# Kernel tuning notes

Measured on AMD Instinct MI355X. Metric: run time of the kernel, lower is better.

The kernel has to match this reference:

```python
import jax, jax.numpy as jnp
import numpy as np

N, E, G = 30000, 240000, 1000
F, H = 78, 10            # in-features, GAT heads
HID = F * H              # 780
NEG_SLOPE = 0.2


def setup_inputs() -> dict:
    key = jax.random.key(0)
    ks = jax.random.split(key, 12)
    x = jax.random.normal(ks[0], (N, F), dtype=jnp.float32)
    edge_index = jax.random.randint(ks[1], (2, E), 0, N, dtype=jnp.int32)
    batch = jnp.sort(jax.random.randint(ks[2], (N,), 0, G, dtype=jnp.int32))
    def lin(k, fan_in, shape):
        return (jax.random.normal(k, shape, dtype=jnp.float32)
                / jnp.sqrt(jnp.float32(fan_in)))
    return {
        "x": x,
        "edge_index": edge_index,
        "batch": batch,
        "W_gat": lin(ks[3], F, (F, HID)),          # GATConv lin weight
        "att_src": lin(ks[4], F, (H, F)),          # GAT attention vectors
        "att_dst": lin(ks[5], F, (H, F)),
        "b_gat": jnp.zeros((HID,), jnp.float32),
        "W_gcn": lin(ks[6], HID, (HID, HID)),
        "b_gcn": jnp.zeros((HID,), jnp.float32),
        "W1": lin(ks[7], 2 * HID, (2 * HID, 1500)),
        "b1": jnp.zeros((1500,), jnp.float32),
        "W2": lin(ks[8], 1500, (1500, 128)),
        "b2": jnp.zeros((128,), jnp.float32),
    }


def _with_self_loops(edge_index):
    loop = jnp.arange(N, dtype=edge_index.dtype)
    src = jnp.concatenate([edge_index[0], loop])
    dst = jnp.concatenate([edge_index[1], loop])
    return src, dst


def reference(x, edge_index, batch, W_gat, att_src, att_dst, b_gat,
              W_gcn, b_gcn, W1, b1, W2, b2):
    src, dst = _with_self_loops(edge_index)  # [E+N]

    # ---- GATConv(78 -> 78, heads=10, concat) ----
    h = (x @ W_gat).reshape(N, H, F)                       # [N,H,F]
    a_src = jnp.einsum('nhf,hf->nh', h, att_src)           # [N,H]
    a_dst = jnp.einsum('nhf,hf->nh', h, att_dst)
    e = jax.nn.leaky_relu(a_src[src] + a_dst[dst], NEG_SLOPE)  # [Et,H]
    # segment softmax over incoming edges of each dst node
    e_max = jax.ops.segment_max(e, dst, num_segments=N)
    e_exp = jnp.exp(e - e_max[dst])
    denom = jax.ops.segment_sum(e_exp, dst, num_segments=N)
    alpha = e_exp / denom[dst]                             # [Et,H]
    msg = h[src] * alpha[:, :, None]                       # [Et,H,F]
    out = jax.ops.segment_sum(msg, dst, num_segments=N).reshape(N, HID) + b_gat
    out = jax.nn.relu(out)

    # ---- GCNConv(780 -> 780), symmetric norm with self loops ----
    h2 = out @ W_gcn                                       # [N,HID]
    deg = jax.ops.segment_sum(jnp.ones_like(dst, jnp.float32), dst,
                              num_segments=N)
    dinv = jax.lax.rsqrt(jnp.maximum(deg, 1.0))
    norm = dinv[src] * dinv[dst]                           # [Et]
    out2 = jax.ops.segment_sum(norm[:, None] * h2[src], dst,
                               num_segments=N) + b_gcn
    out2 = jax.nn.relu(out2)

    # ---- global mean / max pool over molecules ----
    counts = jax.ops.segment_sum(jnp.ones((N,), jnp.float32), batch,
                                 num_segments=G)
    gsum = jax.ops.segment_sum(out2, batch, num_segments=G)
    gmean = gsum / jnp.maximum(counts, 1.0)[:, None]
    gmax = jax.ops.segment_max(out2, batch, num_segments=G)
    gmax = jnp.where(counts[:, None] > 0, gmax, 0.0)
    pooled = jnp.concatenate([gmean, gmax], axis=1)        # [G, 1560]

    # ---- MLP head (dropout = identity at eval) ----
    hidfc = jax.nn.relu(pooled @ W1 + b1)
    return hidfc @ W2 + b2                                 # [G, 128]
```

## Files before the change

### kernel.cpp

```cpp
#include <hip/hip_runtime.h>

#define NN 30000
#define EE 240000
#define ET 270000
#define GG 1000
#define NH 10
#define FF 78
#define HID 780
#define NEG_SLOPE 0.2f

#define LD_H 784
#define KP_GCN 800
#define NP_HID 896
#define KP_X 96
#define MP_N 30080
#define KP_P 1568
#define NP_W1 1536
#define LD_FC 1504
#define MP_G 1024

#define MT 128
#define NT 128
#define KB 32
#define GCH 16
#define NBLK 30

typedef __bf16 bf16_8 __attribute__((ext_vector_type(8)));
typedef float f32x4 __attribute__((ext_vector_type(4)));

__device__ __forceinline__ void async_copy16(const void* g, void* l) {
  __builtin_amdgcn_global_load_lds(
      (const __attribute__((address_space(1))) void*)g,
      (__attribute__((address_space(3))) void*)l, 16, 0, 0);
}

__device__ __forceinline__ float bf2f(unsigned int bits) {
  return __uint_as_float(bits << 16);
}

__global__ void init_kernel(int* __restrict__ cnt, int* __restrict__ fill,
                            int* __restrict__ lo, int* __restrict__ hi) {
  int i = blockIdx.x * blockDim.x + threadIdx.x;
  if (i < NN) { cnt[i] = 0; fill[i] = 0; }
  if (i < GG) { lo[i] = NN; hi[i] = 0; }
}

template <bool OUT_BF>
__global__ __launch_bounds__(256) void mfma_gemm(
    const __bf16* __restrict__ A, const __bf16* __restrict__ BT,
    float* __restrict__ Cf, __bf16* __restrict__ Cb,
    const float* __restrict__ bias, int M, int Kp, int Nout, int ldc,
    int relu, int rp, int nct, int mtiles) {
  __shared__ __bf16 As[4][MT][8];
  __shared__ __bf16 Bs[4][NT][8];
  int rt, ct;
  if (rp > 0) {
    int bid = blockIdx.x;
    int p = bid & 7, s = bid >> 3;
    int q = s / nct;
    rt = p * rp + q;
    ct = s - q * nct;
    if (rt >= mtiles) return;
  } else {
    rt = blockIdx.y; ct = blockIdx.x;
  }
  int row0 = rt * MT, col0 = ct * NT;
  int tid = threadIdx.x;
  int lane = tid & 63, wave = tid >> 6;
  int wm = (wave & 1) * 64, wn = (wave >> 1) * 64;
  int l15 = lane & 15, quad = lane >> 4;
  f32x4 acc[4][4] = {};

  for (int k0 = 0; k0 < Kp; k0 += KB) {
    for (int t = 0; t < 2; t++) {
      int base = t * 256 + wave * 64;
      int s = base + lane;
      int kc = s >> 7, r = s & 127;
      const __bf16* g = A + (size_t)(row0 + r) * Kp + k0 + kc * 8;
      char* l = (char*)&As[0][0][0] + (size_t)base * 16;
      async_copy16(g, l);
    }
    for (int t = 0; t < 2; t++) {
      int base = t * 256 + wave * 64;
      int s = base + lane;
      int kc = s >> 7, r = s & 127;
      const __bf16* g = BT + (size_t)(col0 + r) * Kp + k0 + kc * 8;
      char* l = (char*)&Bs[0][0][0] + (size_t)base * 16;
      async_copy16(g, l);
    }
    __syncthreads();

    bf16_8 af[4], bfv[4];
    for (int mt = 0; mt < 4; mt++)
      af[mt] = *(const bf16_8*)&As[quad][wm + mt * 16 + l15][0];
    for (int nt = 0; nt < 4; nt++)
      bfv[nt] = *(const bf16_8*)&Bs[quad][wn + nt * 16 + l15][0];
    for (int mt = 0; mt < 4; mt++)
      for (int nt = 0; nt < 4; nt++)
        acc[mt][nt] = __builtin_amdgcn_mfma_f32_16x16x32_bf16(
            af[mt], bfv[nt], acc[mt][nt], 0, 0, 0);
    __syncthreads();
  }

  for (int nt = 0; nt < 4; nt++) {
    int col = col0 + wn + nt * 16 + l15;
    if (col >= ldc) continue;
    bool valid = col < Nout;
    float bv = (valid && bias) ? bias[col] : 0.f;
    for (int mt = 0; mt < 4; mt++) {
      int rbase = row0 + wm + mt * 16 + quad * 4;
      for (int r = 0; r < 4; r++) {
        int row = rbase + r;
        if (row >= M) continue;
        float v = 0.f;
        if (valid) {
          v = acc[mt][nt][r] + bv;
          if (relu) v = fmaxf(v, 0.f);
        }
        if (OUT_BF) Cb[(size_t)row * ldc + col] = (__bf16)v;
        else        Cf[(size_t)row * ldc + col] = v;
      }
    }
  }
}

__global__ void wconvT_kernel(const float* __restrict__ W,
                              __bf16* __restrict__ BT, int K, int N, int Kp,
                              int Np) {
  int i = blockIdx.x * blockDim.x + threadIdx.x;
  if (i >= Np * Kp) return;
  int n = i / Kp, k = i - n * Kp;
  BT[i] = (__bf16)((n < N && k < K) ? W[(size_t)k * N + n] : 0.f);
}

__global__ void xconv_kernel(const float* __restrict__ x,
                             __bf16* __restrict__ xb) {
  int i = blockIdx.x * blockDim.x + threadIdx.x;
  if (i >= MP_N * KP_X) return;
  int n = i / KP_X, k = i - n * KP_X;
  xb[i] = (__bf16)((n < NN && k < FF) ? x[(size_t)n * FF + k] : 0.f);
}

__global__ void wsd_kernel(const float* __restrict__ W_gat,
                           const float* __restrict__ att_src,
                           const float* __restrict__ att_dst,
                           float* __restrict__ wsd) {
  int i = blockIdx.x * blockDim.x + threadIdx.x;
  if (i >= FF * 2 * NH) return;
  int k = i / (2 * NH), c = i - k * (2 * NH);
  int h = (c < NH) ? c : c - NH;
  const float* att = (c < NH) ? att_src : att_dst;
  float s = 0.f;
  for (int f = 0; f < FF; f++)
    s += W_gat[(size_t)k * HID + h * FF + f] * att[h * FF + f];
  wsd[k * 2 * NH + c] = s;
}

__global__ __launch_bounds__(256) void adot_kernel(
    const float* __restrict__ x, const float* __restrict__ wsd,
    float* __restrict__ a_src, float* __restrict__ a_dst) {
  __shared__ float w_s[FF * 2 * NH];
  for (int i = threadIdx.x; i < FF * 2 * NH; i += 256) w_s[i] = wsd[i];
  __syncthreads();
  int gid = blockIdx.x * 256 + threadIdx.x;
  if (gid >= NN * 2 * NH) return;
  int n = gid / (2 * NH), c = gid - n * (2 * NH);
  float s = 0.f;
  for (int k = 0; k < FF; k++) s += x[(size_t)n * FF + k] * w_s[k * 2 * NH + c];
  if (c < NH) a_src[n * NH + c] = s;
  else        a_dst[n * NH + (c - NH)] = s;
}

__device__ __forceinline__ void edge_sd(const int* __restrict__ ei, int t,
                                        int& s, int& d) {
  if (t < EE) { s = ei[t]; d = ei[EE + t]; }
  else        { s = t - EE; d = t - EE; }
}

__global__ void count_kernel(const int* __restrict__ ei,
                             const int* __restrict__ batch,
                             int* __restrict__ cnt, int* __restrict__ lo,
                             int* __restrict__ hi) {
  int t = blockIdx.x * blockDim.x + threadIdx.x;
  if (t < ET) { int s, d; edge_sd(ei, t, s, d); atomicAdd(&cnt[d], 1); }
  if (t < NN) {
    int g = batch[t];
    atomicMin(&lo[g], t);
    atomicMax(&hi[g], t + 1);
  }
}

__global__ __launch_bounds__(1024) void scan1_kernel(
    const int* __restrict__ cnt, int* __restrict__ row_ptr,
    int* __restrict__ partial) {
  __shared__ int buf[1024];
  int i = blockIdx.x * 1024 + threadIdx.x;
  int v = (i < NN) ? cnt[i] : 0;
  buf[threadIdx.x] = v;
  __syncthreads();
  for (int off = 1; off < 1024; off <<= 1) {
    int t = (threadIdx.x >= off) ? buf[threadIdx.x - off] : 0;
    __syncthreads();
    buf[threadIdx.x] += t;
    __syncthreads();
  }
  if (i < NN) row_ptr[i] = buf[threadIdx.x] - v;
  if (threadIdx.x == 1023) partial[blockIdx.x] = buf[1023];
}

__global__ void scan2_kernel(int* __restrict__ partial,
                             int* __restrict__ offs) {
  if (threadIdx.x == 0) {
    int run = 0;
    for (int b = 0; b < NBLK; b++) { offs[b] = run; run += partial[b]; }
  }
}

__global__ void scan3_kernel(int* __restrict__ row_ptr,
                             const int* __restrict__ offs,
                             const int* __restrict__ cnt,
                             float* __restrict__ dinv) {
  int i = blockIdx.x * blockDim.x + threadIdx.x;
  if (i < NN) {
    row_ptr[i] += offs[i >> 10];
    dinv[i] = rsqrtf((float)max(cnt[i], 1));
  }
  if (i == 0) row_ptr[NN] = ET;
}

__global__ void scatter_kernel(const int* __restrict__ ei,
                               const int* __restrict__ row_ptr,
                               int* __restrict__ fill,
                               const float* __restrict__ a_src,
                               const float* __restrict__ a_dst,
                               int* __restrict__ col_src,
                               float* __restrict__ p_csr) {
  int t = blockIdx.x * blockDim.x + threadIdx.x;
  if (t >= ET) return;
  int s, d; edge_sd(ei, t, s, d);
  int pos = row_ptr[d] + atomicAdd(&fill[d], 1);
  col_src[pos] = s;
#pragma unroll
  for (int h = 0; h < NH; h++) {
    float v = a_src[s * NH + h] + a_dst[d * NH + h];
    v = (v > 0.f) ? v : v * NEG_SLOPE;
    p_csr[(size_t)pos * NH + h] = __expf(v);
  }
}

__global__ __launch_bounds__(128) void gat_aggr_kernel(
    const int* __restrict__ row_ptr, const int* __restrict__ col_src,
    const float* __restrict__ p_csr, const __bf16* __restrict__ h_bf,
    const float* __restrict__ b_gat, __bf16* __restrict__ A_bf) {
  int d = blockIdx.x;
  int beg = row_ptr[d], end = row_ptr[d + 1];
  int tid = threadIdx.x;
  __shared__ float sum_s[NH];
  __shared__ float al_s[GCH][NH];
  __shared__ int src_s[GCH];
  if (tid < NH) sum_s[tid] = 0.f;
  __syncthreads();

  int f0 = 8 * tid;
  int h0 = f0 / FF; if (h0 > NH - 1) h0 = NH - 1;
  int split = (h0 + 1) * FF - f0; if (split > 8) split = 8;
  int h1 = (h0 < NH - 1) ? h0 + 1 : NH - 1;
  float acc[8] = {};

  for (int c = beg; c < end; c += GCH) {
    int ce = min(GCH, end - c);
    if (tid < ce) src_s[tid] = col_src[c + tid];
    for (int i = tid; i < ce * NH; i += 128) {
      int j = i / NH, h = i - j * NH;
      float p = p_csr[(size_t)(c + j) * NH + h];
      al_s[j][h] = p;
      atomicAdd(&sum_s[h], p);
    }
    __syncthreads();
    if (tid < 98) {
      for (int j = 0; j < ce; j++) {
        uint4 r = *(const uint4*)(h_bf + (size_t)src_s[j] * LD_H + f0);
        float a0 = al_s[j][h0], a1 = al_s[j][h1];
        unsigned int w[4] = {r.x, r.y, r.z, r.w};
#pragma unroll
        for (int k = 0; k < 8; k++) {
          unsigned int bits = (k & 1) ? (w[k >> 1] >> 16) : (w[k >> 1] & 0xffffu);
          acc[k] += bf2f(bits) * ((k < split) ? a0 : a1);
        }
      }
    }
    __syncthreads();
  }
  if (tid < 100) {
    float inv0 = 0.f, inv1 = 0.f;
    if (tid < 98) { inv0 = 1.f / sum_s[h0]; inv1 = 1.f / sum_s[h1]; }
    bf16_8 ov;
#pragma unroll
    for (int k = 0; k < 8; k++) {
      int f = f0 + k;
      float val = 0.f;
      if (tid < 98 && f < HID)
        val = fmaxf(acc[k] * ((k < split) ? inv0 : inv1) + b_gat[f], 0.f);
      ov[k] = (__bf16)val;
    }
    *(bf16_8*)(A_bf + (size_t)d * KP_GCN + f0) = ov;
  }
}

__global__ __launch_bounds__(128) void gcn_aggr_kernel(
    const int* __restrict__ row_ptr, const int* __restrict__ col_src,
    const float* __restrict__ dinv, const __bf16* __restrict__ h2,
    const float* __restrict__ b_gcn, __bf16* __restrict__ out2) {
  int d = blockIdx.x;
  int beg = row_ptr[d], end = row_ptr[d + 1];
  int tid = threadIdx.x;
  float dv = dinv[d];
  __shared__ float w_s[GCH];
  __shared__ int src_s[GCH];
  int f0 = 8 * tid;
  float acc[8] = {};
  for (int c = beg; c < end; c += GCH) {
    int ce = min(GCH, end - c);
    if (tid < ce) {
      int s = col_src[c + tid];
      src_s[tid] = s;
      w_s[tid] = dinv[s] * dv;
    }
    __syncthreads();
    if (tid < 98) {
      for (int j = 0; j < ce; j++) {
        uint4 r = *(const uint4*)(h2 + (size_t)src_s[j] * LD_H + f0);
        float w = w_s[j];
        unsigned int wb[4] = {r.x, r.y, r.z, r.w};
#pragma unroll
        for (int k = 0; k < 8; k++) {
          unsigned int bits = (k & 1) ? (wb[k >> 1] >> 16) : (wb[k >> 1] & 0xffffu);
          acc[k] += bf2f(bits) * w;
        }
      }
    }
    __syncthreads();
  }
  if (tid < 98) {
    bf16_8 ov;
#pragma unroll
    for (int k = 0; k < 8; k++) {
      int f = f0 + k;
      float val = (f < HID) ? fmaxf(acc[k] + b_gcn[f], 0.f) : 0.f;
      ov[k] = (__bf16)val;
    }
    *(bf16_8*)(out2 + (size_t)d * LD_H + f0) = ov;
  }
}

__global__ __launch_bounds__(832) void pool_kernel(
    const __bf16* __restrict__ out2, const int* __restrict__ lo,
    const int* __restrict__ hi, __bf16* __restrict__ pooled) {
  int g = blockIdx.x;
  int l = lo[g], h = hi[g];
  int f = threadIdx.x;
  if (f >= HID) {
    int pad = f - HID;
    if (pad < KP_P - 2 * HID)
      pooled[(size_t)g * KP_P + 2 * HID + pad] = (__bf16)0.f;
    return;
  }
  float s = 0.f, mx = -1e30f;
  for (int n = l; n < h; n++) {
    float v = (float)out2[(size_t)n * LD_H + f];
    s += v;
    mx = fmaxf(mx, v);
  }
  if (h <= l) { s = 0.f; mx = 0.f; }
  else s = s / (float)(h - l);
  pooled[(size_t)g * KP_P + f] = (__bf16)s;
  pooled[(size_t)g * KP_P + HID + f] = (__bf16)mx;
}

extern "C" void kernel_launch(void* const* d_in, const int* in_sizes, int n_in,
                              void* d_out, int out_size, void* d_ws,
                              size_t ws_size, hipStream_t stream) {
  const float* x        = (const float*)d_in[0];
  const int*   edge_idx = (const int*)d_in[1];
  const int*   batch    = (const int*)d_in[2];
  const float* W_gat    = (const float*)d_in[3];
  const float* att_src  = (const float*)d_in[4];
  const float* att_dst  = (const float*)d_in[5];
  const float* b_gat    = (const float*)d_in[6];
  const float* W_gcn    = (const float*)d_in[7];
  const float* b_gcn    = (const float*)d_in[8];
  const float* W1       = (const float*)d_in[9];
  const float* b1       = (const float*)d_in[10];
  const float* W2       = (const float*)d_in[11];
  const float* b2       = (const float*)d_in[12];
  float* out = (float*)d_out;
  (void)in_sizes; (void)n_in; (void)out_size; (void)ws_size;

  char* ws = (char*)d_ws;
  size_t off = 0;
  auto alloc = [&](size_t bytes) -> void* {
    void* p = ws + off;
    off += (bytes + 255) & ~(size_t)255;
    return p;
  };
  char*  bufR     = (char*)alloc((size_t)MP_N * KP_GCN * 2);
  __bf16* A_bf    = (__bf16*)bufR;
  __bf16* out2b   = (__bf16*)bufR;
  __bf16* h_bf    = (__bf16*)alloc((size_t)MP_N * LD_H * 2);
  __bf16* h2_bf   = (__bf16*)alloc((size_t)MP_N * LD_H * 2);
  __bf16* x_bf    = (__bf16*)alloc((size_t)MP_N * KP_X * 2);
  __bf16* WgatT   = (__bf16*)alloc((size_t)NP_HID * KP_X * 2);
  __bf16* WgcnT   = (__bf16*)alloc((size_t)NP_HID * KP_GCN * 2);
  __bf16* W1T     = (__bf16*)alloc((size_t)NP_W1 * KP_P * 2);
  __bf16* W2T     = (__bf16*)alloc((size_t)128 * LD_FC * 2);
  __bf16* pooled  = (__bf16*)alloc((size_t)MP_G * KP_P * 2);
  __bf16* hidfc   = (__bf16*)alloc((size_t)MP_G * LD_FC * 2);
  float* wsd      = (float*)alloc((size_t)FF * 2 * NH * 4);
  float* a_src_b  = (float*)alloc((size_t)NN * NH * 4);
  float* a_dst_b  = (float*)alloc((size_t)NN * NH * 4);
  float* p_csr    = (float*)alloc((size_t)ET * NH * 4);
  int*   cnt      = (int*)alloc((size_t)NN * 4);
  int*   fill     = (int*)alloc((size_t)NN * 4);
  int*   row_ptr  = (int*)alloc((size_t)(NN + 1) * 4);
  int*   col_src  = (int*)alloc((size_t)ET * 4);
  int*   partial  = (int*)alloc((size_t)NBLK * 4);
  int*   offs     = (int*)alloc((size_t)NBLK * 4);
  int*   lo       = (int*)alloc((size_t)GG * 4);
  int*   hi       = (int*)alloc((size_t)GG * 4);
  float* dinv     = (float*)alloc((size_t)NN * 4);

  init_kernel<<<(NN + 255) / 256, 256, 0, stream>>>(cnt, fill, lo, hi);

  xconv_kernel<<<(MP_N * KP_X + 255) / 256, 256, 0, stream>>>(x, x_bf);
  wconvT_kernel<<<(NP_HID * KP_X + 255) / 256, 256, 0, stream>>>(
      W_gat, WgatT, FF, HID, KP_X, NP_HID);
  wconvT_kernel<<<(NP_HID * KP_GCN + 255) / 256, 256, 0, stream>>>(
      W_gcn, WgcnT, HID, HID, KP_GCN, NP_HID);
  wconvT_kernel<<<(NP_W1 * KP_P + 255) / 256, 256, 0, stream>>>(
      W1, W1T, 2 * HID, 1500, KP_P, NP_W1);
  wconvT_kernel<<<(128 * LD_FC + 255) / 256, 256, 0, stream>>>(
      W2, W2T, 1500, 128, LD_FC, 128);
  wsd_kernel<<<(FF * 2 * NH + 255) / 256, 256, 0, stream>>>(
      W_gat, att_src, att_dst, wsd);

  {
    dim3 grid(NP_HID / NT, MP_N / MT);
    mfma_gemm<true><<<grid, 256, 0, stream>>>(x_bf, WgatT, nullptr, h_bf,
                                              nullptr, NN, KP_X, HID, LD_H, 0,
                                              0, 0, 0);
  }
  adot_kernel<<<(NN * 2 * NH + 255) / 256, 256, 0, stream>>>(x, wsd, a_src_b,
                                                             a_dst_b);

  count_kernel<<<(ET + 255) / 256, 256, 0, stream>>>(edge_idx, batch, cnt, lo,
                                                     hi);
  scan1_kernel<<<NBLK, 1024, 0, stream>>>(cnt, row_ptr, partial);
  scan2_kernel<<<1, 64, 0, stream>>>(partial, offs);
  scan3_kernel<<<(NN + 255) / 256, 256, 0, stream>>>(row_ptr, offs, cnt, dinv);
  scatter_kernel<<<(ET + 255) / 256, 256, 0, stream>>>(
      edge_idx, row_ptr, fill, a_src_b, a_dst_b, col_src, p_csr);

  gat_aggr_kernel<<<NN, 128, 0, stream>>>(row_ptr, col_src, p_csr, h_bf,
                                          b_gat, A_bf);
  {
    mfma_gemm<true><<<dim3(8 * 30 * 7), 256, 0, stream>>>(
        A_bf, WgcnT, nullptr, h2_bf, nullptr, NN, KP_GCN, HID, LD_H, 0,
        30, 7, MP_N / MT);
  }
  gcn_aggr_kernel<<<NN, 128, 0, stream>>>(row_ptr, col_src, dinv, h2_bf,
                                          b_gcn, out2b);

  pool_kernel<<<GG, 832, 0, stream>>>(out2b, lo, hi, pooled);

  {
    dim3 grid(NP_W1 / NT, MP_G / MT);
    mfma_gemm<true><<<grid, 256, 0, stream>>>(pooled, W1T, nullptr, hidfc, b1,
                                              GG, KP_P, 1500, LD_FC, 1,
                                              0, 0, 0);
  }
  {
    dim3 grid(1, MP_G / MT);
    mfma_gemm<false><<<grid, 256, 0, stream>>>(hidfc, W2T, out, nullptr, b2,
                                               GG, LD_FC, 128, 128, 0,
                                               0, 0, 0);
  }
}
```

Measured before the change: 612.1 us.

## Use wave-per-node aggregation, templated GEMM K-tile, and vectorized pooling

The GAT and GCN aggregation kernels now assign one 64-lane wave per destination node, with 16 features per lane. This removes the shared-memory staging, LDS atomics and block-wide barriers of the block-per-node design. The GEMM's K block size becomes a template parameter, and the GCN GEMM uses a 64-wide K step with K padding raised to 832 to halve barrier count. Pooling now reads 8 bf16 values per thread with vector loads. Risks: each lane re-reads p_csr and col_src per edge with lower occupancy per wave, and the larger padded K adds some extra GEMM work.

```diff
diff --git a/kernel.cpp b/kernel.cpp
--- a/kernel.cpp
+++ b/kernel.cpp
@@ -10,7 +10,7 @@
 #define NEG_SLOPE 0.2f
 
 #define LD_H 784
-#define KP_GCN 800
+#define KP_GCN 832
 #define NP_HID 896
 #define KP_X 96
 #define MP_N 30080
@@ -21,8 +21,6 @@
 
 #define MT 128
 #define NT 128
-#define KB 32
-#define GCH 16
 #define NBLK 30
 
 typedef __bf16 bf16_8 __attribute__((ext_vector_type(8)));
@@ -45,14 +43,17 @@
   if (i < GG) { lo[i] = NN; hi[i] = 0; }
 }
 
-template <bool OUT_BF>
+template <bool OUT_BF, int KBC>
 __global__ __launch_bounds__(256) void mfma_gemm(
     const __bf16* __restrict__ A, const __bf16* __restrict__ BT,
     float* __restrict__ Cf, __bf16* __restrict__ Cb,
     const float* __restrict__ bias, int M, int Kp, int Nout, int ldc,
     int relu, int rp, int nct, int mtiles) {
-  __shared__ __bf16 As[4][MT][8];
-  __shared__ __bf16 Bs[4][NT][8];
+  constexpr int NCH = KBC / 8;
+  constexpr int TST = KBC / 16;
+  constexpr int NST = KBC / 32;
+  __shared__ __bf16 As[NCH][MT][8];
+  __shared__ __bf16 Bs[NCH][NT][8];
   int rt, ct;
   if (rp > 0) {
     int bid = blockIdx.x;
@@ -71,34 +72,35 @@
   int l15 = lane & 15, quad = lane >> 4;
   f32x4 acc[4][4] = {};
 
-  for (int k0 = 0; k0 < Kp; k0 += KB) {
-    for (int t = 0; t < 2; t++) {
+  for (int k0 = 0; k0 < Kp; k0 += KBC) {
+    for (int t = 0; t < TST; t++) {
       int base = t * 256 + wave * 64;
       int s = base + lane;
       int kc = s >> 7, r = s & 127;
       const __bf16* g = A + (size_t)(row0 + r) * Kp + k0 + kc * 8;
-      char* l = (char*)&As[0][0][0] + (size_t)base * 16;
-      async_copy16(g, l);
-    }
-    for (int t = 0; t < 2; t++) {
+      async_copy16(g, (char*)&As[0][0][0] + (size_t)base * 16);
+    }
+    for (int t = 0; t < TST; t++) {
       int base = t * 256 + wave * 64;
       int s = base + lane;
       int kc = s >> 7, r = s & 127;
       const __bf16* g = BT + (size_t)(col0 + r) * Kp + k0 + kc * 8;
-      char* l = (char*)&Bs[0][0][0] + (size_t)base * 16;
-      async_copy16(g, l);
+      async_copy16(g, (char*)&Bs[0][0][0] + (size_t)base * 16);
     }
     __syncthreads();
 
-    bf16_8 af[4], bfv[4];
-    for (int mt = 0; mt < 4; mt++)
-      af[mt] = *(const bf16_8*)&As[quad][wm + mt * 16 + l15][0];
-    for (int nt = 0; nt < 4; nt++)
-      bfv[nt] = *(const bf16_8*)&Bs[quad][wn + nt * 16 + l15][0];
-    for (int mt = 0; mt < 4; mt++)
+    bf16_8 af[NST][4], bfv[NST][4];
+    for (int st = 0; st < NST; st++) {
+      for (int mt = 0; mt < 4; mt++)
+        af[st][mt] = *(const bf16_8*)&As[st * 4 + quad][wm + mt * 16 + l15][0];
       for (int nt = 0; nt < 4; nt++)
-        acc[mt][nt] = __builtin_amdgcn_mfma_f32_16x16x32_bf16(
-            af[mt], bfv[nt], acc[mt][nt], 0, 0, 0);
+        bfv[st][nt] = *(const bf16_8*)&Bs[st * 4 + quad][wn + nt * 16 + l15][0];
+    }
+    for (int st = 0; st < NST; st++)
+      for (int mt = 0; mt < 4; mt++)
+        for (int nt = 0; nt < 4; nt++)
+          acc[mt][nt] = __builtin_amdgcn_mfma_f32_16x16x32_bf16(
+              af[st][mt], bfv[st][nt], acc[mt][nt], 0, 0, 0);
     __syncthreads();
   }
 
@@ -248,133 +250,129 @@
   }
 }
 
-__global__ __launch_bounds__(128) void gat_aggr_kernel(
+__global__ __launch_bounds__(256) void gat_aggr_kernel(
     const int* __restrict__ row_ptr, const int* __restrict__ col_src,
     const float* __restrict__ p_csr, const __bf16* __restrict__ h_bf,
     const float* __restrict__ b_gat, __bf16* __restrict__ A_bf) {
-  int d = blockIdx.x;
+  int wave = threadIdx.x >> 6;
+  int lane = threadIdx.x & 63;
+  int d = blockIdx.x * 4 + wave;
   int beg = row_ptr[d], end = row_ptr[d + 1];
-  int tid = threadIdx.x;
-  __shared__ float sum_s[NH];
-  __shared__ float al_s[GCH][NH];
-  __shared__ int src_s[GCH];
-  if (tid < NH) sum_s[tid] = 0.f;
-  __syncthreads();
-
-  int f0 = 8 * tid;
-  int h0 = f0 / FF; if (h0 > NH - 1) h0 = NH - 1;
-  int split = (h0 + 1) * FF - f0; if (split > 8) split = 8;
-  int h1 = (h0 < NH - 1) ? h0 + 1 : NH - 1;
-  float acc[8] = {};
-
-  for (int c = beg; c < end; c += GCH) {
-    int ce = min(GCH, end - c);
-    if (tid < ce) src_s[tid] = col_src[c + tid];
-    for (int i = tid; i < ce * NH; i += 128) {
-      int j = i / NH, h = i - j * NH;
-      float p = p_csr[(size_t)(c + j) * NH + h];
-      al_s[j][h] = p;
-      atomicAdd(&sum_s[h], p);
-    }
-    __syncthreads();
-    if (tid < 98) {
-      for (int j = 0; j < ce; j++) {
-        uint4 r = *(const uint4*)(h_bf + (size_t)src_s[j] * LD_H + f0);
-        float a0 = al_s[j][h0], a1 = al_s[j][h1];
-        unsigned int w[4] = {r.x, r.y, r.z, r.w};
-#pragma unroll
-        for (int k = 0; k < 8; k++) {
-          unsigned int bits = (k & 1) ? (w[k >> 1] >> 16) : (w[k >> 1] & 0xffffu);
-          acc[k] += bf2f(bits) * ((k < split) ? a0 : a1);
-        }
+  int f0 = 16 * lane;
+
+  if (lane < 49) {
+    int h0 = f0 / FF;
+    int split = (h0 + 1) * FF - f0;
+    if (split > 16) split = 16;
+    int h1 = (h0 < NH - 1) ? h0 + 1 : NH - 1;
+    float acc[16] = {};
+    float sum0 = 0.f, sum1 = 0.f;
+    for (int e = beg; e < end; e++) {
+      int s = col_src[e];
+      float p0 = p_csr[(size_t)e * NH + h0];
+      float p1 = p_csr[(size_t)e * NH + h1];
+      sum0 += p0; sum1 += p1;
+      const __bf16* rowp = h_bf + (size_t)s * LD_H + f0;
+      uint4 r0 = *(const uint4*)rowp;
+      uint4 r1 = *(const uint4*)(rowp + 8);
+      unsigned int w[8] = {r0.x, r0.y, r0.z, r0.w, r1.x, r1.y, r1.z, r1.w};
+#pragma unroll
+      for (int k = 0; k < 16; k++) {
+        unsigned int bits = (k & 1) ? (w[k >> 1] >> 16) : (w[k >> 1] & 0xffffu);
+        acc[k] += bf2f(bits) * ((k < split) ? p0 : p1);
       }
     }
-    __syncthreads();
-  }
-  if (tid < 100) {
-    float inv0 = 0.f, inv1 = 0.f;
-    if (tid < 98) { inv0 = 1.f / sum_s[h0]; inv1 = 1.f / sum_s[h1]; }
-    bf16_8 ov;
-#pragma unroll
-    for (int k = 0; k < 8; k++) {
+    float inv0 = 1.f / sum0, inv1 = 1.f / sum1;
+    bf16_8 o0, o1;
+#pragma unroll
+    for (int k = 0; k < 16; k++) {
       int f = f0 + k;
       float val = 0.f;
-      if (tid < 98 && f < HID)
+      if (f < HID)
         val = fmaxf(acc[k] * ((k < split) ? inv0 : inv1) + b_gat[f], 0.f);
-      ov[k] = (__bf16)val;
-    }
-    *(bf16_8*)(A_bf + (size_t)d * KP_GCN + f0) = ov;
-  }
-}
-
-__global__ __launch_bounds__(128) void gcn_aggr_kernel(
+      if (k < 8) o0[k] = (__bf16)val; else o1[k - 8] = (__bf16)val;
+    }
+    *(bf16_8*)(A_bf + (size_t)d * KP_GCN + f0) = o0;
+    *(bf16_8*)(A_bf + (size_t)d * KP_GCN + f0 + 8) = o1;
+  } else if (lane < 52) {
+    bf16_8 z = {};
+    *(bf16_8*)(A_bf + (size_t)d * KP_GCN + f0) = z;
+    *(bf16_8*)(A_bf + (size_t)d * KP_GCN + f0 + 8) = z;
+  }
+}
+
+__global__ __launch_bounds__(256) void gcn_aggr_kernel(
     const int* __restrict__ row_ptr, const int* __restrict__ col_src,
     const float* __restrict__ dinv, const __bf16* __restrict__ h2,
     const float* __restrict__ b_gcn, __bf16* __restrict__ out2) {
-  int d = blockIdx.x;
+  int wave = threadIdx.x >> 6;
+  int lane = threadIdx.x & 63;
+  int d = blockIdx.x * 4 + wave;
   int beg = row_ptr[d], end = row_ptr[d + 1];
-  int tid = threadIdx.x;
+  if (lane >= 49) return;
+  int f0 = 16 * lane;
   float dv = dinv[d];
-  __shared__ float w_s[GCH];
-  __shared__ int src_s[GCH];
-  int f0 = 8 * tid;
-  float acc[8] = {};
-  for (int c = beg; c < end; c += GCH) {
-    int ce = min(GCH, end - c);
-    if (tid < ce) {
-      int s = col_src[c + tid];
-      src_s[tid] = s;
-      w_s[tid] = dinv[s] * dv;
-    }
-    __syncthreads();
-    if (tid < 98) {
-      for (int j = 0; j < ce; j++) {
-        uint4 r = *(const uint4*)(h2 + (size_t)src_s[j] * LD_H + f0);
-        float w = w_s[j];
-        unsigned int wb[4] = {r.x, r.y, r.z, r.w};
-#pragma unroll
-        for (int k = 0; k < 8; k++) {
-          unsigned int bits = (k & 1) ? (wb[k >> 1] >> 16) : (wb[k >> 1] & 0xffffu);
-          acc[k] += bf2f(bits) * w;
-        }
-      }
-    }
-    __syncthreads();
-  }
-  if (tid < 98) {
-    bf16_8 ov;
-#pragma unroll
-    for (int k = 0; k < 8; k++) {
-      int f = f0 + k;
-      float val = (f < HID) ? fmaxf(acc[k] + b_gcn[f], 0.f) : 0.f;
-      ov[k] = (__bf16)val;
-    }
-    *(bf16_8*)(out2 + (size_t)d * LD_H + f0) = ov;
-  }
-}
-
-__global__ __launch_bounds__(832) void pool_kernel(
+  float acc[16] = {};
+  for (int e = beg; e < end; e++) {
+    int s = col_src[e];
+    float w = dinv[s] * dv;
+    const __bf16* rowp = h2 + (size_t)s * LD_H + f0;
+    uint4 r0 = *(const uint4*)rowp;
+    uint4 r1 = *(const uint4*)(rowp + 8);
+    unsigned int wb[8] = {r0.x, r0.y, r0.z, r0.w, r1.x, r1.y, r1.z, r1.w};
+#pragma unroll
+    for (int k = 0; k < 16; k++) {
+      unsigned int bits = (k & 1) ? (wb[k >> 1] >> 16) : (wb[k >> 1] & 0xffffu);
+      acc[k] += bf2f(bits) * w;
+    }
+  }
+  bf16_8 o0, o1;
+#pragma unroll
+  for (int k = 0; k < 16; k++) {
+    int f = f0 + k;
+    float val = (f < HID) ? fmaxf(acc[k] + b_gcn[f], 0.f) : 0.f;
+    if (k < 8) o0[k] = (__bf16)val; else o1[k - 8] = (__bf16)val;
+  }
+  *(bf16_8*)(out2 + (size_t)d * LD_H + f0) = o0;
+  *(bf16_8*)(out2 + (size_t)d * LD_H + f0 + 8) = o1;
+}
+
+__global__ __launch_bounds__(128) void pool_kernel(
     const __bf16* __restrict__ out2, const int* __restrict__ lo,
     const int* __restrict__ hi, __bf16* __restrict__ pooled) {
   int g = blockIdx.x;
   int l = lo[g], h = hi[g];
-  int f = threadIdx.x;
-  if (f >= HID) {
-    int pad = f - HID;
-    if (pad < KP_P - 2 * HID)
-      pooled[(size_t)g * KP_P + 2 * HID + pad] = (__bf16)0.f;
+  int t = threadIdx.x;
+  if (t == 98) {
+    for (int k = 0; k < 8; k++) pooled[(size_t)g * KP_P + 1560 + k] = (__bf16)0.f;
     return;
   }
-  float s = 0.f, mx = -1e30f;
+  if (t >= 98) return;
+  int f0 = 8 * t;
+  float s[8] = {}, mx[8];
+#pragma unroll
+  for (int k = 0; k < 8; k++) mx[k] = -1e30f;
   for (int n = l; n < h; n++) {
-    float v = (float)out2[(size_t)n * LD_H + f];
-    s += v;
-    mx = fmaxf(mx, v);
-  }
-  if (h <= l) { s = 0.f; mx = 0.f; }
-  else s = s / (float)(h - l);
-  pooled[(size_t)g * KP_P + f] = (__bf16)s;
-  pooled[(size_t)g * KP_P + HID + f] = (__bf16)mx;
+    uint4 r = *(const uint4*)(out2 + (size_t)n * LD_H + f0);
+    unsigned int w[4] = {r.x, r.y, r.z, r.w};
+#pragma unroll
+    for (int k = 0; k < 8; k++) {
+      unsigned int bits = (k & 1) ? (w[k >> 1] >> 16) : (w[k >> 1] & 0xffffu);
+      float v = bf2f(bits);
+      s[k] += v;
+      mx[k] = fmaxf(mx[k], v);
+    }
+  }
+  float invc = (h > l) ? 1.f / (float)(h - l) : 0.f;
+#pragma unroll
+  for (int k = 0; k < 8; k++) {
+    int f = f0 + k;
+    if (f >= HID) continue;
+    float mean = (h > l) ? s[k] * invc : 0.f;
+    float mxx  = (h > l) ? mx[k] : 0.f;
+    pooled[(size_t)g * KP_P + f] = (__bf16)mean;
+    pooled[(size_t)g * KP_P + HID + f] = (__bf16)mxx;
+  }
 }
 
 extern "C" void kernel_launch(void* const* d_in, const int* in_sizes, int n_in,
@@ -445,9 +443,8 @@
 
   {
     dim3 grid(NP_HID / NT, MP_N / MT);
-    mfma_gemm<true><<<grid, 256, 0, stream>>>(x_bf, WgatT, nullptr, h_bf,
-                                              nullptr, NN, KP_X, HID, LD_H, 0,
-                                              0, 0, 0);
+    mfma_gemm<true, 32><<<grid, 256, 0, stream>>>(
+        x_bf, WgatT, nullptr, h_bf, nullptr, NN, KP_X, HID, LD_H, 0, 0, 0, 0);
   }
   adot_kernel<<<(NN * 2 * NH + 255) / 256, 256, 0, stream>>>(x, wsd, a_src_b,
                                                              a_dst_b);
@@ -460,28 +457,26 @@
   scatter_kernel<<<(ET + 255) / 256, 256, 0, stream>>>(
       edge_idx, row_ptr, fill, a_src_b, a_dst_b, col_src, p_csr);
 
-  gat_aggr_kernel<<<NN, 128, 0, stream>>>(row_ptr, col_src, p_csr, h_bf,
-                                          b_gat, A_bf);
+  gat_aggr_kernel<<<NN / 4, 256, 0, stream>>>(row_ptr, col_src, p_csr, h_bf,
+                                              b_gat, A_bf);
   {
-    mfma_gemm<true><<<dim3(8 * 30 * 7), 256, 0, stream>>>(
+    mfma_gemm<true, 64><<<dim3(8 * 30 * 7), 256, 0, stream>>>(
         A_bf, WgcnT, nullptr, h2_bf, nullptr, NN, KP_GCN, HID, LD_H, 0,
         30, 7, MP_N / MT);
   }
-  gcn_aggr_kernel<<<NN, 128, 0, stream>>>(row_ptr, col_src, dinv, h2_bf,
-                                          b_gcn, out2b);
-
-  pool_kernel<<<GG, 832, 0, stream>>>(out2b, lo, hi, pooled);
+  gcn_aggr_kernel<<<NN / 4, 256, 0, stream>>>(row_ptr, col_src, dinv, h2_bf,
+                                              b_gcn, out2b);
+
+  pool_kernel<<<GG, 128, 0, stream>>>(out2b, lo, hi, pooled);
 
   {
     dim3 grid(NP_W1 / NT, MP_G / MT);
-    mfma_gemm<true><<<grid, 256, 0, stream>>>(pooled, W1T, nullptr, hidfc, b1,
-                                              GG, KP_P, 1500, LD_FC, 1,
-                                              0, 0, 0);
+    mfma_gemm<true, 32><<<grid, 256, 0, stream>>>(
+        pooled, W1T, nullptr, hidfc, b1, GG, KP_P, 1500, LD_FC, 1, 0, 0, 0);
   }
   {
     dim3 grid(1, MP_G / MT);
-    mfma_gemm<false><<<grid, 256, 0, stream>>>(hidfc, W2T, out, nullptr, b2,
-                                               GG, LD_FC, 128, 128, 0,
-                                               0, 0, 0);
-  }
-}
+    mfma_gemm<false, 32><<<grid, 256, 0, stream>>>(
+        hidfc, W2T, out, nullptr, b2, GG, LD_FC, 128, 128, 0, 0, 0, 0);
+  }
+}
```

New measurement: 631.2 us. 3.1% more time.
